# Kernel tuning notes

Hardware: AMD Instinct MI355X
Metric: run time of the kernel (lower is better)

## Reference

```python
import jax, jax.numpy as jnp
import numpy as np


def _resize_bilinear_align_corners(x, out_size):
    # x: [B, C, h, w] -> [B, C, out_size, out_size], matches F.interpolate(mode='bilinear', align_corners=True)
    def axis_interp(arr, size_in, size_out, axis):
        coords = jnp.linspace(0.0, size_in - 1.0, size_out)
        i0 = jnp.floor(coords).astype(jnp.int32)
        i1 = jnp.minimum(i0 + 1, size_in - 1)
        t = (coords - i0).astype(arr.dtype)
        a0 = jnp.take(arr, i0, axis=axis)
        a1 = jnp.take(arr, i1, axis=axis)
        shape = [1] * arr.ndim
        shape[axis] = size_out
        t = t.reshape(shape)
        return a0 * (1.0 - t) + a1 * t

    B, C, h, w = x.shape
    x = axis_interp(x, h, out_size, 2)
    x = axis_interp(x, w, out_size, 3)
    return x


def _similarity_matrix(x, sp, num):
    # Torch: mean_values[i][j] = mean(x[i][sp_repeated[i] == j], dim=0)
    # Boolean indexing flattens across channels, so this is a SCALAR mean over
    # (channels x segment pixels), broadcast to all C channels.
    B, C, H, W = x.shape
    xs = x.sum(axis=1).reshape(B, H * W)          # sum over channels, per pixel
    ids = sp.reshape(B, H * W)
    seg_sum = jax.vmap(
        lambda v, i: jax.ops.segment_sum(v, i, num_segments=num))(xs, ids)
    cnt = jax.vmap(
        lambda i: jax.ops.segment_sum(jnp.ones(i.shape, x.dtype), i,
                                      num_segments=num))(ids)
    m = seg_sum / (cnt * C)                        # [B, num] scalar mean per segment
    # diff vector over channels has identical entries -> norm(diff)/sqrt(C) == |m_i - m_j|
    return 1.0 - jnp.abs(m[:, :, None] - m[:, None, :])  # [B, num, num]


def reference(input, feature, sp, num):
    feature = _resize_bilinear_align_corners(feature, input.shape[-1])
    mat1 = _similarity_matrix(input, sp, num)
    mat2 = _similarity_matrix(feature, sp, num)
    return jnp.mean(jnp.abs(mat1 - mat2))


def setup_inputs() -> dict:
    key = jax.random.key(0)
    k1, k2, k3 = jax.random.split(key, 3)
    B, C_in, H, W = 8, 64, 256, 256
    C_feat, hf, wf = 256, 64, 64
    num = 256
    return {
        "input": jax.random.normal(k1, (B, C_in, H, W), dtype=jnp.float32),
        "feature": jax.random.normal(k2, (B, C_feat, hf, wf), dtype=jnp.float32),
        "sp": jax.random.randint(k3, (B, 1, H, W), 0, num, dtype=jnp.int32),
        "num": num,
    }
```

## Files before the change

kernel.cpp:

```cpp
#include <hip/hip_runtime.h>

#define NB 8
#define C_IN 64
#define HW 65536
#define CF 256
#define FHW 4096
#define NSEG 256
#define FBLK 16
#define MBLK 64
#define MAGIC 0x13579BDFu


__global__ __launch_bounds__(256) void k1(
    const float* __restrict__ input, const int* __restrict__ sp,
    const float* __restrict__ feat,
    float* __restrict__ fsum, float* __restrict__ seg_part) {
  __shared__ float smem[1024];
  int b = blockIdx.y, t = threadIdx.x;

  if (blockIdx.x < FBLK) {
    int e = blockIdx.x;
    int q = t & 63, cg = t >> 6;
    const float4* f4 = (const float4*)(feat + (size_t)b * CF * FHW);
    int col = e * 64 + q;
    float4 s = make_float4(0.f, 0.f, 0.f, 0.f);
#pragma unroll 8
    for (int c = cg; c < CF; c += 4) {
      float4 v = f4[(size_t)c * (FHW / 4) + col];
      s.x += v.x; s.y += v.y; s.z += v.z; s.w += v.w;
    }
    float4* lred = (float4*)smem;
    lred[cg * 64 + q] = s;
    __syncthreads();
    if (t < 64) {
      float4 a = lred[t], b1 = lred[64 + t], c1 = lred[128 + t], d = lred[192 + t];
      a.x += b1.x + c1.x + d.x; a.y += b1.y + c1.y + d.y;
      a.z += b1.z + c1.z + d.z; a.w += b1.w + c1.w + d.w;
      ((float4*)fsum)[(size_t)b * (FHW / 4) + e * 64 + t] = a;
    }
    return;
  }

  int blk = blockIdx.x - FBLK;
  float* bin_x = smem;
  float* bin_c = smem + NSEG;
  bin_x[t] = 0.f; bin_c[t] = 0.f;
  __syncthreads();
  int v0 = blk * 256 + t;
  const float4* in4 = (const float4*)(input + (size_t)b * C_IN * HW);
  float4 xs = make_float4(0.f, 0.f, 0.f, 0.f);
#pragma unroll
  for (int c = 0; c < C_IN; ++c) {
    float4 v = in4[(size_t)c * (HW / 4) + v0];
    xs.x += v.x; xs.y += v.y; xs.z += v.z; xs.w += v.w;
  }
  int4 sv = ((const int4*)(sp + (size_t)b * HW))[v0];
  atomicAdd(&bin_x[sv.x], xs.x); atomicAdd(&bin_c[sv.x], 1.f);
  atomicAdd(&bin_x[sv.y], xs.y); atomicAdd(&bin_c[sv.y], 1.f);
  atomicAdd(&bin_x[sv.z], xs.z); atomicAdd(&bin_c[sv.z], 1.f);
  atomicAdd(&bin_x[sv.w], xs.w); atomicAdd(&bin_c[sv.w], 1.f);
  __syncthreads();
  float* sb = seg_part + (size_t)(b * MBLK + blk) * 2 * NSEG;
  sb[t] = bin_x[t];
  sb[NSEG + t] = bin_c[t];
}

__global__ __launch_bounds__(256) void k2(
    const int* __restrict__ sp, const float* __restrict__ fsum,
    float* __restrict__ binf_part) {
  __shared__ float fls[FHW];
  __shared__ float binf[NSEG];
  int e = blockIdx.x, b = blockIdx.y, t = threadIdx.x;
  {
    const float4* s4 = (const float4*)(fsum + (size_t)b * FHW);
    float4* d4 = (float4*)fls;
#pragma unroll
    for (int i = 0; i < 4; ++i) d4[i * 256 + t] = s4[i * 256 + t];
  }
  binf[t] = 0.f;
  __syncthreads();
  const int4* sp4 = (const int4*)(sp + (size_t)b * HW);
#pragma unroll
  for (int k = 0; k < 8; ++k) {
    int v4 = e * 2048 + k * 256 + t;
    int4 sv = sp4[v4];
    int p0 = v4 * 4;
    int y = p0 >> 8;
    float cy = (float)y * (63.0f / 255.0f);
    int iy = (int)cy; float ty = cy - (float)iy; int iy1 = min(iy + 1, 63);
    int svv[4] = {sv.x, sv.y, sv.z, sv.w};
#pragma unroll
    for (int kk = 0; kk < 4; ++kk) {
      int x = (p0 + kk) & 255;
      float cx = (float)x * (63.0f / 255.0f);
      int ix = (int)cx; float tx = cx - (float)ix; int ix1 = min(ix + 1, 63);
      float f00 = fls[iy * 64 + ix],  f10 = fls[iy1 * 64 + ix];
      float f01 = fls[iy * 64 + ix1], f11 = fls[iy1 * 64 + ix1];
      float a0 = f00 * (1.f - ty) + f10 * ty;
      float a1 = f01 * (1.f - ty) + f11 * ty;
      atomicAdd(&binf[svv[kk]], a0 * (1.f - tx) + a1 * tx);
    }
  }
  __syncthreads();
  binf_part[(size_t)(b * 8 + e) * NSEG + t] = binf[t];
}

__global__ __launch_bounds__(1024) void k3(
    const float* __restrict__ seg_part, const float* __restrict__ binf_part,
    unsigned* __restrict__ ppbits, unsigned* __restrict__ bflags,
    float* __restrict__ out) {
  __shared__ float s2[2 * NSEG];
  __shared__ float sf[NSEG];
  __shared__ float m1[NSEG], m2[NSEG];
  __shared__ float red[16];
  int b = blockIdx.x, t = threadIdx.x;
  if (t < 2 * NSEG) {
    const float* base = seg_part + (size_t)b * MBLK * 2 * NSEG + t;
    float s = 0.f;
#pragma unroll
    for (int k = 0; k < MBLK; ++k) s += base[k * 2 * NSEG];
    s2[t] = s;
  } else if (t < 2 * NSEG + NSEG) {
    int u = t - 2 * NSEG;
    const float* base = binf_part + (size_t)b * 8 * NSEG + u;
    float s = 0.f;
#pragma unroll
    for (int k = 0; k < 8; ++k) s += base[k * NSEG];
    sf[u] = s;
  }
  __syncthreads();
  if (t < NSEG) {
    float cnt = s2[NSEG + t];
    m1[t] = s2[t] / (cnt * 64.0f);
    m2[t] = sf[t] / (cnt * 256.0f);
  }
  __syncthreads();
  int i = t & 255, j0 = (t >> 8) * 64;
  float a1 = m1[i], a2 = m2[i], acc = 0.f;
#pragma unroll
  for (int jj = 0; jj < 64; ++jj) {
    int j = j0 + jj;
    acc += fabsf(fabsf(a1 - m1[j]) - fabsf(a2 - m2[j]));
  }
#pragma unroll
  for (int off = 32; off; off >>= 1) acc += __shfl_down(acc, off);
  if ((t & 63) == 0) red[t >> 6] = acc;
  __syncthreads();
  if (t == 0) {
    float s = 0.f;
#pragma unroll
    for (int w = 0; w < 16; ++w) s += red[w];
    __hip_atomic_store(&ppbits[b], __float_as_uint(s), __ATOMIC_RELAXED,
                       __HIP_MEMORY_SCOPE_AGENT);
    __hip_atomic_store(&bflags[b], MAGIC, __ATOMIC_RELEASE,
                       __HIP_MEMORY_SCOPE_AGENT);
    if (b == 0) {
      float tot = s;
      for (int ob = 1; ob < NB; ++ob) {
        while (__hip_atomic_load(&bflags[ob], __ATOMIC_ACQUIRE,
                                 __HIP_MEMORY_SCOPE_AGENT) != MAGIC) {}
        tot += __uint_as_float(__hip_atomic_load(
            &ppbits[ob], __ATOMIC_RELAXED, __HIP_MEMORY_SCOPE_AGENT));
      }
      out[0] = tot / 524288.0f;
      for (int ob = 0; ob < NB; ++ob)
        __hip_atomic_store(&bflags[ob], 0u, __ATOMIC_RELAXED,
                           __HIP_MEMORY_SCOPE_AGENT);
    }
  }
}

extern "C" void kernel_launch(void* const* d_in, const int* in_sizes, int n_in,
                              void* d_out, int out_size, void* d_ws, size_t ws_size,
                              hipStream_t stream) {
  const float* input   = (const float*)d_in[0];
  const float* feature = (const float*)d_in[1];
  const int*   sp      = (const int*)d_in[2];
  float* ws = (float*)d_ws;
  float*    fsum      = ws;
  float*    seg_part  = ws + (size_t)NB * FHW;
  float*    binf_part = seg_part + (size_t)NB * MBLK * 2 * NSEG;
  unsigned* ppbits    = (unsigned*)(binf_part + (size_t)NB * 8 * NSEG);
  unsigned* bflags    = ppbits + NB;

  k1<<<dim3(FBLK + MBLK, NB), 256, 0, stream>>>(input, sp, feature, fsum, seg_part);
  k2<<<dim3(8, NB), 256, 0, stream>>>(sp, fsum, binf_part);
  k3<<<dim3(NB), 1024, 0, stream>>>(seg_part, binf_part, ppbits, bflags,
                                    (float*)d_out);
}
```

Measured before the change: 53.36 us.

## Fuse three kernels into one persistent launch with per-batch flag barriers

Merges the channel-sum, bilinear-resize segment accumulation and final pairwise reduction into a single kernel launch. Blocks coordinate through global memory flags: the feature-sum blocks publish completion, block 0 of each batch releases the segment blocks, and those blocks then do the resize accumulation for their own pixel slice before block 0 reduces everything. The aim is to remove launch gaps and inter-kernel drains. In exchange it depends on all 640 blocks being co-resident, since spin-waiting blocks could otherwise deadlock, and it adds flag traffic plus a larger 64-way partial reduction.

```diff
diff --git a/kernel.cpp b/kernel.cpp
--- a/kernel.cpp
+++ b/kernel.cpp
@@ -8,83 +8,64 @@
 #define NSEG 256
 #define FBLK 16
 #define MBLK 64
+#define TOTB 80
 #define MAGIC 0x13579BDFu
-
-
-__global__ __launch_bounds__(256) void k1(
+#define AG __HIP_MEMORY_SCOPE_AGENT
+
+
+__global__ __launch_bounds__(256) void fused(
     const float* __restrict__ input, const int* __restrict__ sp,
     const float* __restrict__ feat,
-    float* __restrict__ fsum, float* __restrict__ seg_part) {
-  __shared__ float smem[1024];
-  int b = blockIdx.y, t = threadIdx.x;
-
-  if (blockIdx.x < FBLK) {
-    int e = blockIdx.x;
-    int q = t & 63, cg = t >> 6;
-    const float4* f4 = (const float4*)(feat + (size_t)b * CF * FHW);
-    int col = e * 64 + q;
-    float4 s = make_float4(0.f, 0.f, 0.f, 0.f);
-#pragma unroll 8
-    for (int c = cg; c < CF; c += 4) {
-      float4 v = f4[(size_t)c * (FHW / 4) + col];
-      s.x += v.x; s.y += v.y; s.z += v.z; s.w += v.w;
-    }
-    float4* lred = (float4*)smem;
-    lred[cg * 64 + q] = s;
-    __syncthreads();
-    if (t < 64) {
-      float4 a = lred[t], b1 = lred[64 + t], c1 = lred[128 + t], d = lred[192 + t];
-      a.x += b1.x + c1.x + d.x; a.y += b1.y + c1.y + d.y;
-      a.z += b1.z + c1.z + d.z; a.w += b1.w + c1.w + d.w;
-      ((float4*)fsum)[(size_t)b * (FHW / 4) + e * 64 + t] = a;
-    }
-    return;
-  }
-
-  int blk = blockIdx.x - FBLK;
-  float* bin_x = smem;
-  float* bin_c = smem + NSEG;
-  bin_x[t] = 0.f; bin_c[t] = 0.f;
-  __syncthreads();
-  int v0 = blk * 256 + t;
-  const float4* in4 = (const float4*)(input + (size_t)b * C_IN * HW);
-  float4 xs = make_float4(0.f, 0.f, 0.f, 0.f);
-#pragma unroll
-  for (int c = 0; c < C_IN; ++c) {
-    float4 v = in4[(size_t)c * (HW / 4) + v0];
-    xs.x += v.x; xs.y += v.y; xs.z += v.z; xs.w += v.w;
-  }
-  int4 sv = ((const int4*)(sp + (size_t)b * HW))[v0];
-  atomicAdd(&bin_x[sv.x], xs.x); atomicAdd(&bin_c[sv.x], 1.f);
-  atomicAdd(&bin_x[sv.y], xs.y); atomicAdd(&bin_c[sv.y], 1.f);
-  atomicAdd(&bin_x[sv.z], xs.z); atomicAdd(&bin_c[sv.z], 1.f);
-  atomicAdd(&bin_x[sv.w], xs.w); atomicAdd(&bin_c[sv.w], 1.f);
-  __syncthreads();
-  float* sb = seg_part + (size_t)(b * MBLK + blk) * 2 * NSEG;
-  sb[t] = bin_x[t];
-  sb[NSEG + t] = bin_c[t];
-}
-
-__global__ __launch_bounds__(256) void k2(
-    const int* __restrict__ sp, const float* __restrict__ fsum,
-    float* __restrict__ binf_part) {
-  __shared__ float fls[FHW];
-  __shared__ float binf[NSEG];
-  int e = blockIdx.x, b = blockIdx.y, t = threadIdx.x;
-  {
-    const float4* s4 = (const float4*)(fsum + (size_t)b * FHW);
-    float4* d4 = (float4*)fls;
-#pragma unroll
-    for (int i = 0; i < 4; ++i) d4[i * 256 + t] = s4[i * 256 + t];
-  }
-  binf[t] = 0.f;
-  __syncthreads();
-  const int4* sp4 = (const int4*)(sp + (size_t)b * HW);
-#pragma unroll
-  for (int k = 0; k < 8; ++k) {
-    int v4 = e * 2048 + k * 256 + t;
-    int4 sv = sp4[v4];
-    int p0 = v4 * 4;
+    float* __restrict__ fsum, float* __restrict__ seg_part,
+    float* __restrict__ binf_part,
+    unsigned* __restrict__ p1, unsigned* __restrict__ p2,
+    unsigned* __restrict__ r1, unsigned* __restrict__ ppbits,
+    unsigned* __restrict__ bflags, float* __restrict__ out) {
+  __shared__ float smem[FHW + NSEG];
+  int b = blockIdx.y, e = blockIdx.x, t = threadIdx.x;
+
+  if (e >= FBLK) {
+    int blk = e - FBLK;
+    float* bin_x = smem;
+    float* bin_c = smem + NSEG;
+    bin_x[t] = 0.f; bin_c[t] = 0.f;
+    __syncthreads();
+    int v0 = blk * 256 + t;
+    const float4* in4 = (const float4*)(input + (size_t)b * C_IN * HW);
+    float4 xs = make_float4(0.f, 0.f, 0.f, 0.f);
+#pragma unroll
+    for (int c = 0; c < C_IN; ++c) {
+      float4 v = in4[(size_t)c * (HW / 4) + v0];
+      xs.x += v.x; xs.y += v.y; xs.z += v.z; xs.w += v.w;
+    }
+    int4 sv = ((const int4*)(sp + (size_t)b * HW))[v0];
+    atomicAdd(&bin_x[sv.x], xs.x); atomicAdd(&bin_c[sv.x], 1.f);
+    atomicAdd(&bin_x[sv.y], xs.y); atomicAdd(&bin_c[sv.y], 1.f);
+    atomicAdd(&bin_x[sv.z], xs.z); atomicAdd(&bin_c[sv.z], 1.f);
+    atomicAdd(&bin_x[sv.w], xs.w); atomicAdd(&bin_c[sv.w], 1.f);
+    __syncthreads();
+    float* sb = seg_part + (size_t)(b * MBLK + blk) * 2 * NSEG;
+    sb[t] = bin_x[t];
+    sb[NSEG + t] = bin_c[t];
+    __syncthreads();
+    if (t == 0) {
+      __hip_atomic_store(&p1[b * TOTB + e], MAGIC, __ATOMIC_RELEASE, AG);
+      while (__hip_atomic_load(&r1[b], __ATOMIC_RELAXED, AG) != MAGIC)
+        __builtin_amdgcn_s_sleep(2);
+    }
+    __syncthreads();
+    __builtin_amdgcn_fence(__ATOMIC_ACQUIRE, "agent");
+    {
+      const float4* s4 = (const float4*)(fsum + (size_t)b * FHW);
+      float4* d4 = (float4*)smem;
+#pragma unroll
+      for (int i = 0; i < 4; ++i) d4[i * 256 + t] = s4[i * 256 + t];
+    }
+    float* fls = smem;
+    float* binf = smem + FHW;
+    binf[t] = 0.f;
+    __syncthreads();
+    int p0 = v0 * 4;
     int y = p0 >> 8;
     float cy = (float)y * (63.0f / 255.0f);
     int iy = (int)cy; float ty = cy - (float)iy; int iy1 = min(iy + 1, 63);
@@ -100,72 +81,109 @@
       float a1 = f01 * (1.f - ty) + f11 * ty;
       atomicAdd(&binf[svv[kk]], a0 * (1.f - tx) + a1 * tx);
     }
-  }
-  __syncthreads();
-  binf_part[(size_t)(b * 8 + e) * NSEG + t] = binf[t];
-}
-
-__global__ __launch_bounds__(1024) void k3(
-    const float* __restrict__ seg_part, const float* __restrict__ binf_part,
-    unsigned* __restrict__ ppbits, unsigned* __restrict__ bflags,
-    float* __restrict__ out) {
-  __shared__ float s2[2 * NSEG];
-  __shared__ float sf[NSEG];
-  __shared__ float m1[NSEG], m2[NSEG];
-  __shared__ float red[16];
-  int b = blockIdx.x, t = threadIdx.x;
-  if (t < 2 * NSEG) {
-    const float* base = seg_part + (size_t)b * MBLK * 2 * NSEG + t;
+    __syncthreads();
+    binf_part[(size_t)(b * MBLK + blk) * NSEG + t] = binf[t];
+    __syncthreads();
+    if (t == 0)
+      __hip_atomic_store(&p2[b * MBLK + blk], MAGIC, __ATOMIC_RELEASE, AG);
+    return;
+  }
+
+  {
+    int q = t & 63, cg = t >> 6;
+    const float4* f4 = (const float4*)(feat + (size_t)b * CF * FHW);
+    int col = e * 64 + q;
+    float4 s = make_float4(0.f, 0.f, 0.f, 0.f);
+#pragma unroll 8
+    for (int c = cg; c < CF; c += 4) {
+      float4 v = f4[(size_t)c * (FHW / 4) + col];
+      s.x += v.x; s.y += v.y; s.z += v.z; s.w += v.w;
+    }
+    float4* lred = (float4*)smem;
+    lred[cg * 64 + q] = s;
+    __syncthreads();
+    if (t < 64) {
+      float4 a = lred[t], b1 = lred[64 + t], c1 = lred[128 + t], d = lred[192 + t];
+      a.x += b1.x + c1.x + d.x; a.y += b1.y + c1.y + d.y;
+      a.z += b1.z + c1.z + d.z; a.w += b1.w + c1.w + d.w;
+      ((float4*)fsum)[(size_t)b * (FHW / 4) + e * 64 + t] = a;
+    }
+    __syncthreads();
+  }
+  if (e != 0) {
+    if (t == 0)
+      __hip_atomic_store(&p1[b * TOTB + e], MAGIC, __ATOMIC_RELEASE, AG);
+    return;
+  }
+
+  if (t >= 1 && t < TOTB) {
+    unsigned* f = &p1[b * TOTB + t];
+    while (__hip_atomic_load(f, __ATOMIC_RELAXED, AG) != MAGIC)
+      __builtin_amdgcn_s_sleep(2);
+    __hip_atomic_store(f, 0u, __ATOMIC_RELAXED, AG);
+  }
+  __syncthreads();
+  if (t == 0)
+    __hip_atomic_store(&r1[b], MAGIC, __ATOMIC_RELEASE, AG);
+  if (t < MBLK) {
+    unsigned* f = &p2[b * MBLK + t];
+    while (__hip_atomic_load(f, __ATOMIC_RELAXED, AG) != MAGIC)
+      __builtin_amdgcn_s_sleep(2);
+    __hip_atomic_store(f, 0u, __ATOMIC_RELAXED, AG);
+  }
+  __syncthreads();
+  __builtin_amdgcn_fence(__ATOMIC_ACQUIRE, "agent");
+  if (t == 0) __hip_atomic_store(&r1[b], 0u, __ATOMIC_RELAXED, AG);
+
+  float* s2 = smem;
+  float* sf = smem + 512;
+  float* m1 = smem + 768;
+  float* m2 = smem + 1024;
+  float* red = smem + 1280;
+  for (int u = t; u < 2 * NSEG; u += 256) {
+    const float* base = seg_part + (size_t)b * MBLK * 2 * NSEG + u;
     float s = 0.f;
 #pragma unroll
     for (int k = 0; k < MBLK; ++k) s += base[k * 2 * NSEG];
-    s2[t] = s;
-  } else if (t < 2 * NSEG + NSEG) {
-    int u = t - 2 * NSEG;
-    const float* base = binf_part + (size_t)b * 8 * NSEG + u;
+    s2[u] = s;
+  }
+  {
+    const float* base = binf_part + (size_t)b * MBLK * NSEG + t;
     float s = 0.f;
 #pragma unroll
-    for (int k = 0; k < 8; ++k) s += base[k * NSEG];
-    sf[u] = s;
-  }
-  __syncthreads();
-  if (t < NSEG) {
+    for (int k = 0; k < MBLK; ++k) s += base[k * NSEG];
+    sf[t] = s;
+  }
+  __syncthreads();
+  {
     float cnt = s2[NSEG + t];
     m1[t] = s2[t] / (cnt * 64.0f);
     m2[t] = sf[t] / (cnt * 256.0f);
   }
   __syncthreads();
-  int i = t & 255, j0 = (t >> 8) * 64;
-  float a1 = m1[i], a2 = m2[i], acc = 0.f;
-#pragma unroll
-  for (int jj = 0; jj < 64; ++jj) {
-    int j = j0 + jj;
+  float a1 = m1[t], a2 = m2[t], acc = 0.f;
+#pragma unroll 8
+  for (int j = 0; j < NSEG; ++j)
     acc += fabsf(fabsf(a1 - m1[j]) - fabsf(a2 - m2[j]));
-  }
 #pragma unroll
   for (int off = 32; off; off >>= 1) acc += __shfl_down(acc, off);
   if ((t & 63) == 0) red[t >> 6] = acc;
   __syncthreads();
   if (t == 0) {
-    float s = 0.f;
-#pragma unroll
-    for (int w = 0; w < 16; ++w) s += red[w];
-    __hip_atomic_store(&ppbits[b], __float_as_uint(s), __ATOMIC_RELAXED,
-                       __HIP_MEMORY_SCOPE_AGENT);
-    __hip_atomic_store(&bflags[b], MAGIC, __ATOMIC_RELEASE,
-                       __HIP_MEMORY_SCOPE_AGENT);
+    float s = red[0] + red[1] + red[2] + red[3];
+    __hip_atomic_store(&ppbits[b], __float_as_uint(s), __ATOMIC_RELAXED, AG);
+    __hip_atomic_store(&bflags[b], MAGIC, __ATOMIC_RELEASE, AG);
     if (b == 0) {
       float tot = s;
       for (int ob = 1; ob < NB; ++ob) {
-        while (__hip_atomic_load(&bflags[ob], __ATOMIC_ACQUIRE,
-                                 __HIP_MEMORY_SCOPE_AGENT) != MAGIC) {}
+        while (__hip_atomic_load(&bflags[ob], __ATOMIC_RELAXED, AG) != MAGIC)
+          __builtin_amdgcn_s_sleep(2);
         tot += __uint_as_float(__hip_atomic_load(
-            &ppbits[ob], __ATOMIC_RELAXED, __HIP_MEMORY_SCOPE_AGENT));
+            &ppbits[ob], __ATOMIC_RELAXED, AG));
+        __hip_atomic_store(&bflags[ob], 0u, __ATOMIC_RELAXED, AG);
       }
       out[0] = tot / 524288.0f;
-      for (int ob = 0; ob < NB; ++ob)
-        __hip_atomic_store(&bflags[ob], 0u, __ATOMIC_RELAXED,
-                           __HIP_MEMORY_SCOPE_AGENT);
+      __hip_atomic_store(&bflags[0], 0u, __ATOMIC_RELAXED, AG);
     }
   }
 }
@@ -180,11 +198,14 @@
   float*    fsum      = ws;
   float*    seg_part  = ws + (size_t)NB * FHW;
   float*    binf_part = seg_part + (size_t)NB * MBLK * 2 * NSEG;
-  unsigned* ppbits    = (unsigned*)(binf_part + (size_t)NB * 8 * NSEG);
-  unsigned* bflags    = ppbits + NB;
-
-  k1<<<dim3(FBLK + MBLK, NB), 256, 0, stream>>>(input, sp, feature, fsum, seg_part);
-  k2<<<dim3(8, NB), 256, 0, stream>>>(sp, fsum, binf_part);
-  k3<<<dim3(NB), 1024, 0, stream>>>(seg_part, binf_part, ppbits, bflags,
-                                    (float*)d_out);
+  unsigned* ub        = (unsigned*)(binf_part + (size_t)NB * MBLK * NSEG);
+  unsigned* p1     = ub;
+  unsigned* p2     = p1 + NB * TOTB;
+  unsigned* r1     = p2 + NB * MBLK;
+  unsigned* ppbits = r1 + NB;
+  unsigned* bflags = ppbits + NB;
+
+  fused<<<dim3(TOTB, NB), 256, 0, stream>>>(input, sp, feature, fsum, seg_part,
+                                            binf_part, p1, p2, r1, ppbits,
+                                            bflags, (float*)d_out);
 }
```

New measurement: 79.66 us. 1.49x slower.
